# Kernel tuning notes

Hardware: AMD Instinct MI355X
Metric: run time of the kernel (lower is better)

The kernel has to match this reference:

```python
import jax, jax.numpy as jnp
import numpy as np

N = 100000
E = 1600000
NFEAT, NHID1, NHID2, NCLASS, NSTRUC = 512, 256, 128, 40, 128


def glorot(key, shape):
    lim = 1.0 / np.sqrt(shape[0])
    return jax.random.uniform(key, shape, jnp.float32, -lim, lim)


def setup_inputs() -> dict:
    key = jax.random.key(0)
    ks = jax.random.split(key, 12)
    x = jax.random.normal(ks[0], (N, NFEAT), jnp.float32)
    edge_index = jax.random.randint(ks[1], (2, E), 0, N, jnp.int32)
    edge_weight = jax.random.uniform(ks[2], (E,), jnp.float32)
    return {
        "x": x,
        "edge_index": edge_index,
        "edge_weight": edge_weight,
        "W1": glorot(ks[3], (NFEAT, NHID1)), "b1": jnp.zeros((NHID1,), jnp.float32),
        "W2": glorot(ks[4], (NHID1, NHID2)), "b2": jnp.zeros((NHID2,), jnp.float32),
        "W3": glorot(ks[5], (NHID2, NCLASS)), "b3": jnp.zeros((NCLASS,), jnp.float32),
        "We": glorot(ks[6], (NHID1, NSTRUC)), "be": jnp.zeros((NSTRUC,), jnp.float32),
    }


def spmm(edge_index, edge_weight, support):
    # adj @ support with adj given as weighted edge list (dst <- src)
    src, dst = edge_index[0], edge_index[1]
    msgs = support[src] * edge_weight[:, None]  # [E, d]
    return jax.ops.segment_sum(msgs, dst, num_segments=N)


def gc_layer(x, edge_index, edge_weight, W, b):
    support = x @ W
    return spmm(edge_index, edge_weight, support) + b


def reference(x, edge_index, edge_weight, W1, b1, W2, b2, W3, b3, We, be):
    # eval mode: dropout is identity
    h = jax.nn.relu(gc_layer(x, edge_index, edge_weight, W1, b1))
    out1 = jax.nn.relu(gc_layer(h, edge_index, edge_weight, W2, b2))
    out1 = gc_layer(out1, edge_index, edge_weight, W3, b3)
    out2 = h @ We + be
    return jax.nn.log_softmax(out1, axis=1), out2
```

## Files before the change

### kernel.cpp

```cpp
#include <hip/hip_runtime.h>
#include <hip/hip_bf16.h>

#define NNODES 100000
#define NEDGES 1600000
#define BSH 7
#define NBUCK ((NNODES + 127) >> 7)
#define SPBLK 1536
#define P4CHUNK 8192
#define NSCAT ((NEDGES + P4CHUNK - 1) / P4CHUNK)
#define MH1 391

typedef __attribute__((ext_vector_type(8))) short bf16x8;
typedef __attribute__((ext_vector_type(4))) short bf16x4;
typedef __attribute__((ext_vector_type(2))) short bf16x2;
typedef __attribute__((ext_vector_type(4))) float f32x4;
typedef __attribute__((ext_vector_type(2))) float f32x2;

static __device__ __forceinline__ short f2bf(float f) {
  __hip_bfloat16 b = __float2bfloat16(f);
  return __builtin_bit_cast(short, b);
}
static __device__ __forceinline__ float bf2f(short s) {
  unsigned int u = ((unsigned int)(unsigned short)s) << 16;
  return __builtin_bit_cast(float, u);
}
static __device__ __forceinline__ void fma4(f32x4& a, float w, bf16x4 v) {
  a[0] = fmaf(w, bf2f(v[0]), a[0]);
  a[1] = fmaf(w, bf2f(v[1]), a[1]);
  a[2] = fmaf(w, bf2f(v[2]), a[2]);
  a[3] = fmaf(w, bf2f(v[3]), a[3]);
}
static __device__ __forceinline__ void fma2(f32x2& a, float w, bf16x2 v) {
  a[0] = fmaf(w, bf2f(v[0]), a[0]);
  a[1] = fmaf(w, bf2f(v[1]), a[1]);
}

static __device__ __forceinline__ void gload16(const void* g, void* l) {
  __builtin_amdgcn_global_load_lds(
      (const __attribute__((address_space(1))) unsigned int*)g,
      (__attribute__((address_space(3))) unsigned int*)l, 16, 0, 0);
}

static __device__ __forceinline__ void wtrans_body(int blk, const float* __restrict__ W,
                                                   short* __restrict__ Wt,
                                                   int K, int Nvalid, int Npad) {
  int idx = blk * 256 + threadIdx.x;
  if (idx >= Npad * K) return;
  int n = idx / K, k = idx - n * K;
  int ks = (k & ~63) | ((((k >> 3) & 7) ^ (n & 7)) << 3) | (k & 7);
  Wt[idx] = (n < Nvalid) ? f2bf(W[(size_t)ks * Nvalid + n]) : (short)0;
}

static __device__ __forceinline__ void bcount_body(int blk, const int* __restrict__ ei,
                                                   int* __restrict__ bcnt, int* h) {
  for (int i = threadIdx.x; i < NBUCK; i += 256) h[i] = 0;
  __syncthreads();
  for (int e = blk * 256 + threadIdx.x; e < NEDGES; e += 256 * 256)
    atomicAdd(&h[ei[NEDGES + e] >> BSH], 1);
  __syncthreads();
  for (int i = threadIdx.x; i < NBUCK; i += 256)
    if (h[i]) atomicAdd(&bcnt[i], h[i]);
}

static __device__ __forceinline__ void bscatter_body(int blk, int* cnt, int* pos,
                                                     const int* __restrict__ ei,
                                                     const float* __restrict__ ew,
                                                     int* __restrict__ bcur,
                                                     int2* __restrict__ tmp) {
  int tid = threadIdx.x;
  for (int i = tid; i < NBUCK; i += 256) cnt[i] = 0;
  __syncthreads();
  int base = blk * P4CHUNK;
  int end = base + P4CHUNK;
  if (end > NEDGES) end = NEDGES;
  for (int e = base + tid; e < end; e += 256)
    atomicAdd(&cnt[ei[NEDGES + e] >> BSH], 1);
  __syncthreads();
  for (int i = tid; i < NBUCK; i += 256)
    if (cnt[i]) pos[i] = atomicAdd(&bcur[i], cnt[i]);
  __syncthreads();
  for (int e = base + tid; e < end; e += 256) {
    int d = ei[NEDGES + e];
    int b = d >> BSH;
    int p = atomicAdd(&pos[b], 1);
    tmp[p] = make_int2(ei[e] | ((d & 127) << 17), __float_as_int(ew[e]));
  }
}

static __device__ __forceinline__ void bsort_body(int b, int* hist, int* cur,
                                                  const int* __restrict__ bbase,
                                                  const int2* __restrict__ tmp,
                                                  int2* __restrict__ edat,
                                                  int* __restrict__ rowptr) {
  int tid = threadIdx.x;
  int base = bbase[b], cnt = bbase[b + 1] - base;
  if (tid < 128) hist[tid] = 0;
  __syncthreads();
  for (int i = tid; i < cnt; i += 256)
    atomicAdd(&hist[(tmp[base + i].x >> 17) & 127], 1);
  __syncthreads();
  int c = (tid < 128) ? hist[tid] : 0;
  if (tid < 128) cur[tid] = c;
  __syncthreads();
  for (int off = 1; off < 128; off <<= 1) {
    int v = (tid < 128 && tid >= off) ? cur[tid - off] : 0;
    __syncthreads();
    if (tid < 128) cur[tid] += v;
    __syncthreads();
  }
  if (tid < 128) {
    int ex = cur[tid] - c;
    int node = (b << BSH) + tid;
    if (node < NNODES) rowptr[node] = base + ex;
    cur[tid] = base + ex;
  }
  __syncthreads();
  for (int i = tid; i < cnt; i += 256) {
    int2 r = tmp[base + i];
    int d = (r.x >> 17) & 127;
    int p = atomicAdd(&cur[d], 1);
    edat[p] = make_int2(r.x & 0x1FFFF, r.y);
  }
}

__global__ void bscan_kernel(const int* __restrict__ bcnt, int* __restrict__ bbase,
                             int* __restrict__ bcur, int* __restrict__ rowptr) {
  __shared__ int lds[1024];
  int t = threadIdx.x;
  int c = (t < NBUCK) ? bcnt[t] : 0;
  lds[t] = c;
  __syncthreads();
  for (int off = 1; off < 1024; off <<= 1) {
    int v = (t >= off) ? lds[t - off] : 0;
    __syncthreads();
    lds[t] += v;
    __syncthreads();
  }
  if (t < NBUCK) {
    int ex = lds[t] - c;
    bbase[t] = ex;
    bcur[t] = ex;
  }
  if (t == NBUCK) bbase[t] = NEDGES;
  if (t == 0) rowptr[NNODES] = NEDGES;
}

#define LDSTR 72
template <bool AF32, int EPI>
static __device__ void gemm_body(int my, int nx, short* As, short* Bs,
                                 const void* __restrict__ Aptr, int K,
                                 const short* __restrict__ Wt,
                                 void* __restrict__ Cp0, float* __restrict__ Cp1,
                                 const float* __restrict__ bias, int nvalid, int ldc) {
  int tid = threadIdx.x;
  int lane = tid & 63, wv = tid >> 6;
  int wr = wv >> 1, wc = wv & 1;
  int m0 = my * 128;
  int n0 = nx * 128;
  f32x4 acc[4][4];
#pragma unroll
  for (int i = 0; i < 4; i++)
#pragma unroll
    for (int j = 0; j < 4; j++) acc[i][j] = (f32x4){0.f, 0.f, 0.f, 0.f};

  int srow = tid >> 3;
  int scol = (tid & 7) * 8;

  for (int k0 = 0; k0 < K; k0 += 64) {
    if constexpr (AF32) {
#pragma unroll
      for (int p = 0; p < 4; p++) {
        int ml = p * 32 + srow;
        int arow = m0 + ml;
        if (arow >= NNODES) arow = NNODES - 1;
        const float* ap = (const float*)Aptr + (size_t)arow * K + k0 + scol;
        f32x4 a0 = *(const f32x4*)ap;
        f32x4 a1 = *(const f32x4*)(ap + 4);
        bf16x8 av;
#pragma unroll
        for (int j = 0; j < 4; j++) { av[j] = f2bf(a0[j]); av[4 + j] = f2bf(a1[j]); }
        *(bf16x8*)&As[ml * LDSTR + scol] = av;
      }
    } else {
#pragma unroll
      for (int p = 0; p < 4; p++) {
        int row = p * 32 + wv * 8 + (lane >> 3);
        int arow = m0 + row;
        if (arow >= NNODES) arow = NNODES - 1;
        gload16((const short*)Aptr + (size_t)arow * K + k0 + (lane & 7) * 8,
                &As[p * 2048 + wv * 512]);
      }
    }
#pragma unroll
    for (int p = 0; p < 4; p++) {
      int row = p * 32 + wv * 8 + (lane >> 3);
      gload16(Wt + (size_t)(n0 + row) * K + k0 + (lane & 7) * 8,
              &Bs[p * 2048 + wv * 512]);
    }
    __syncthreads();
    int r = lane & 15, quad = lane >> 4;
#pragma unroll
    for (int kk = 0; kk < 64; kk += 32) {
      int csw = (kk + quad * 8) ^ ((r & 7) << 3);
      bf16x8 af[4], bfr[4];
#pragma unroll
      for (int i = 0; i < 4; i++) {
        if constexpr (AF32)
          af[i] = *(const bf16x8*)&As[(wr * 64 + i * 16 + r) * LDSTR + kk + quad * 8];
        else
          af[i] = *(const bf16x8*)&As[((wr * 64 + i * 16 + r) << 6) + csw];
      }
#pragma unroll
      for (int j = 0; j < 4; j++)
        bfr[j] = *(const bf16x8*)&Bs[((wc * 64 + j * 16 + r) << 6) + csw];
#pragma unroll
      for (int i = 0; i < 4; i++)
#pragma unroll
        for (int j = 0; j < 4; j++)
          acc[i][j] = __builtin_amdgcn_mfma_f32_16x16x32_bf16(af[i], bfr[j], acc[i][j], 0, 0, 0);
    }
    __syncthreads();
  }

  int quad = lane >> 4, cl = lane & 15;
#pragma unroll
  for (int i = 0; i < 4; i++) {
    int rowb = m0 + wr * 64 + i * 16 + quad * 4;
#pragma unroll
    for (int rr = 0; rr < 4; rr++) {
      int row = rowb + rr;
      if (row < NNODES) {
#pragma unroll
        for (int j = 0; j < 4; j++) {
          int col = n0 + wc * 64 + j * 16 + cl;
          float v = acc[i][j][rr];
          if (EPI == 0) {
            ((short*)Cp0)[(size_t)row * ldc + col] = f2bf(v);
          } else if (EPI == 1) {
            if (col < nvalid) Cp1[(size_t)row * nvalid + col] = v;
          } else {
            if (col < 128) ((short*)Cp0)[(size_t)row * 128 + col] = f2bf(v);
            else Cp1[(size_t)row * 128 + (col - 128)] = v + bias[col - 128];
          }
        }
      }
    }
  }
}

template <bool AF32, int EPI>
__launch_bounds__(256, 2)
__global__ void gemm_tiled(const void* __restrict__ Aptr, int K,
                           const short* __restrict__ Wt,
                           void* __restrict__ Cp0, float* __restrict__ Cp1,
                           const float* __restrict__ bias, int nvalid, int ldc) {
  __shared__ __align__(16) short As[128 * (AF32 ? LDSTR : 64)];
  __shared__ __align__(16) short Bs[128 * 64];
  gemm_body<AF32, EPI>(blockIdx.y, blockIdx.x, As, Bs, Aptr, K, Wt, Cp0, Cp1, bias, nvalid, ldc);
}

__launch_bounds__(256)
__global__ void front_kernel(const float* __restrict__ W1, short* __restrict__ Wt1,
                             const float* __restrict__ W2, const float* __restrict__ We,
                             short* __restrict__ Wt2e, const float* __restrict__ W3,
                             short* __restrict__ Wt3,
                             const int* __restrict__ ei, int* __restrict__ bcnt) {
  __shared__ int h[NBUCK];
  int b = blockIdx.x;
  if (b < 256) { bcount_body(b, ei, bcnt, h); return; }
  b -= 256;
  if (b < 512) { wtrans_body(b, W1, Wt1, 512, 256, 256); return; }
  b -= 512;
  if (b < 128) { wtrans_body(b, W2, Wt2e, 256, 128, 128); return; }
  b -= 128;
  if (b < 128) { wtrans_body(b, We, Wt2e + (size_t)128 * 256, 256, 128, 128); return; }
  b -= 128;
  wtrans_body(b, W3, Wt3, 128, 40, 128);
}
#define FRONT_BLOCKS (256 + 512 + 128 + 128 + 64)

__launch_bounds__(256, 2)
__global__ void fuseA_kernel(const int* __restrict__ ei, const float* __restrict__ ew,
                             int* __restrict__ bcur, int2* __restrict__ tmp,
                             const float* __restrict__ x, const short* __restrict__ Wt1,
                             short* __restrict__ S1bf) {
  __shared__ __align__(16) short As[128 * LDSTR];
  __shared__ __align__(16) short Bs[128 * 64];
  __shared__ int sc_cnt[NBUCK];
  __shared__ int sc_pos[NBUCK];
  if (blockIdx.x < NSCAT) {
    bscatter_body(blockIdx.x, sc_cnt, sc_pos, ei, ew, bcur, tmp);
  } else {
    int g = blockIdx.x - NSCAT;
    gemm_body<true, 0>(g >> 1, g & 1, As, Bs, x, 512, Wt1, S1bf, nullptr, nullptr, 256, 256);
  }
}

__launch_bounds__(256, 2)
__global__ void fuseB_kernel(const int* __restrict__ bbase, const int2* __restrict__ tmp,
                             int2* __restrict__ edat, int* __restrict__ rowptr,
                             const float* __restrict__ x, const short* __restrict__ Wt1,
                             short* __restrict__ S1bf) {
  __shared__ __align__(16) short As[128 * LDSTR];
  __shared__ __align__(16) short Bs[128 * 64];
  __shared__ int so_hist[128];
  __shared__ int so_cur[128];
  if (blockIdx.x < NBUCK) {
    bsort_body(blockIdx.x, so_hist, so_cur, bbase, tmp, edat, rowptr);
  } else {
    int g = blockIdx.x - NBUCK;
    gemm_body<true, 0>(MH1 + (g >> 1), g & 1, As, Bs, x, 512, Wt1, S1bf, nullptr, nullptr, 256, 256);
  }
}


template <int NE>
static __device__ __forceinline__ void gat1(int2 me, int b, const short* Sc,
                                            f32x4& acc0, f32x4& acc1) {
  int src[NE]; float wt[NE]; bf16x4 v[NE];
#pragma unroll
  for (int j = 0; j < NE; j++) {
    src[j] = __builtin_amdgcn_readlane(me.x, b + j);
    wt[j] = __builtin_bit_cast(float, __builtin_amdgcn_readlane(me.y, b + j));
  }
#pragma unroll
  for (int j = 0; j < NE; j++) v[j] = *(const bf16x4*)(Sc + (size_t)src[j] * 256);
#pragma unroll
  for (int j = 0; j < NE; j++) {
    if (j & 1) fma4(acc1, wt[j], v[j]); else fma4(acc0, wt[j], v[j]);
  }
}

template <int NE>
static __device__ __forceinline__ void gat2(int2 me, int b, const short* Sc,
                                            f32x2& acc0, f32x2& acc1) {
  int src[NE]; float wt[NE]; bf16x2 v[NE];
#pragma unroll
  for (int j = 0; j < NE; j++) {
    src[j] = __builtin_amdgcn_readlane(me.x, b + j);
    wt[j] = __builtin_bit_cast(float, __builtin_amdgcn_readlane(me.y, b + j));
  }
#pragma unroll
  for (int j = 0; j < NE; j++) v[j] = *(const bf16x2*)(Sc + (size_t)src[j] * 128);
#pragma unroll
  for (int j = 0; j < NE; j++) {
    if (j & 1) fma2(acc1, wt[j], v[j]); else fma2(acc0, wt[j], v[j]);
  }
}

template <int NE>
static __device__ __forceinline__ void gat3(int2 me, int b, const float* S3l,
                                            float& acc0, float& acc1) {
  int src[NE]; float wt[NE]; float v[NE];
#pragma unroll
  for (int j = 0; j < NE; j++) {
    src[j] = __builtin_amdgcn_readlane(me.x, b + j);
    wt[j] = __builtin_bit_cast(float, __builtin_amdgcn_readlane(me.y, b + j));
  }
#pragma unroll
  for (int j = 0; j < NE; j++) v[j] = S3l[(size_t)src[j] * 40];
#pragma unroll
  for (int j = 0; j < NE; j++) {
    if (j & 1) acc1 = fmaf(wt[j], v[j], acc1); else acc0 = fmaf(wt[j], v[j], acc0);
  }
}

__launch_bounds__(256, 6)
__global__ void spmm1_kernel(const int* __restrict__ rowptr, const int2* __restrict__ edat,
                             const short* __restrict__ S,
                             const float* __restrict__ bias, short* __restrict__ H) {
  int nw = gridDim.x * 4;
  int wid = blockIdx.x * 4 + (threadIdx.x >> 6);
  int lane = threadIdx.x & 63;
  int c0 = lane * 4;
  const short* Sc = S + c0;
  f32x4 bv = *(const f32x4*)(bias + c0);
  for (int node = wid; node < NNODES; node += nw) {
    f32x4 acc0 = (f32x4){0.f, 0.f, 0.f, 0.f};
    f32x4 acc1 = (f32x4){0.f, 0.f, 0.f, 0.f};
    int beg = rowptr[node], end = rowptr[node + 1];
    for (int w0 = beg; w0 < end; w0 += 64) {
      int wcnt = end - w0;
      if (wcnt > 64) wcnt = 64;
      int2 me = (lane < wcnt) ? edat[w0 + lane] : make_int2(0, 0);
      int g16 = wcnt >> 4, rem = wcnt & 15;
      int b = 0;
      for (int g = 0; g < g16; ++g, b += 16) gat1<16>(me, b, Sc, acc0, acc1);
      if (rem) {
        if (rem > 8) gat1<16>(me, b, Sc, acc0, acc1);
        else gat1<8>(me, b, Sc, acc0, acc1);
      }
    }
    bf16x4 h;
#pragma unroll
    for (int j = 0; j < 4; j++) h[j] = f2bf(fmaxf(acc0[j] + acc1[j] + bv[j], 0.f));
    int c0w = ((lane >> 4) << 6) + ((((lane >> 1) & 7) ^ (node & 7)) << 3) + ((lane & 1) << 2);
    *(bf16x4*)(H + (size_t)node * 256 + c0w) = h;
  }
}

__launch_bounds__(256, 6)
__global__ void spmm2_kernel(const int* __restrict__ rowptr, const int2* __restrict__ edat,
                             const short* __restrict__ S,
                             const float* __restrict__ bias, short* __restrict__ H) {
  int nw = gridDim.x * 4;
  int wid = blockIdx.x * 4 + (threadIdx.x >> 6);
  int lane = threadIdx.x & 63;
  int c0 = lane * 2;
  const short* Sc = S + c0;
  float b0 = bias[c0], b1 = bias[c0 + 1];
  for (int node = wid; node < NNODES; node += nw) {
    f32x2 acc0 = (f32x2){0.f, 0.f};
    f32x2 acc1 = (f32x2){0.f, 0.f};
    int beg = rowptr[node], end = rowptr[node + 1];
    for (int w0 = beg; w0 < end; w0 += 64) {
      int wcnt = end - w0;
      if (wcnt > 64) wcnt = 64;
      int2 me = (lane < wcnt) ? edat[w0 + lane] : make_int2(0, 0);
      int g16 = wcnt >> 4, rem = wcnt & 15;
      int b = 0;
      for (int g = 0; g < g16; ++g, b += 16) gat2<16>(me, b, Sc, acc0, acc1);
      if (rem) {
        if (rem > 8) gat2<16>(me, b, Sc, acc0, acc1);
        else gat2<8>(me, b, Sc, acc0, acc1);
      }
    }
    bf16x2 h;
    h[0] = f2bf(fmaxf(acc0[0] + acc1[0] + b0, 0.f));
    h[1] = f2bf(fmaxf(acc0[1] + acc1[1] + b1, 0.f));
    int c0w = ((lane >> 5) << 6) + ((((lane >> 2) & 7) ^ (node & 7)) << 3) + ((lane & 3) << 1);
    *(bf16x2*)(H + (size_t)node * 128 + c0w) = h;
  }
}

__launch_bounds__(256, 6)
__global__ void spmm3_kernel(const int* __restrict__ rowptr, const int2* __restrict__ edat,
                             const float* __restrict__ S3,
                             const float* __restrict__ b3, float* __restrict__ out1) {
  int nw = gridDim.x * 4;
  int wid = blockIdx.x * 4 + (threadIdx.x >> 6);
  int lane = threadIdx.x & 63;
  bool act = lane < 40;
  const float* S3l = S3 + lane;
  float bl = act ? b3[lane] : 0.f;
  for (int node = wid; node < NNODES; node += nw) {
    float acc0 = 0.f, acc1 = 0.f;
    int beg = rowptr[node], end = rowptr[node + 1];
    for (int w0 = beg; w0 < end; w0 += 64) {
      int wcnt = end - w0;
      if (wcnt > 64) wcnt = 64;
      int2 me = (lane < wcnt) ? edat[w0 + lane] : make_int2(0, 0);
      int g16 = wcnt >> 4, rem = wcnt & 15;
      int b = 0;
      for (int g = 0; g < g16; ++g, b += 16) gat3<16>(me, b, S3l, acc0, acc1);
      if (rem) {
        if (rem > 8) gat3<16>(me, b, S3l, acc0, acc1);
        else gat3<8>(me, b, S3l, acc0, acc1);
      }
    }
    float acc = acc0 + acc1 + bl;
    float v = act ? acc : -__builtin_inff();
    for (int off = 32; off > 0; off >>= 1) v = fmaxf(v, __shfl_xor(v, off));
    float e = act ? expf(acc - v) : 0.f;
    for (int off = 32; off > 0; off >>= 1) e += __shfl_xor(e, off);
    float ls = logf(e);
    if (act) out1[(size_t)node * 40 + lane] = acc - v - ls;
  }
}

extern "C" void kernel_launch(void* const* d_in, const int* in_sizes, int n_in,
                              void* d_out, int out_size, void* d_ws, size_t ws_size,
                              hipStream_t stream) {
  const float* x  = (const float*)d_in[0];
  const int*   ei = (const int*)d_in[1];
  const float* ew = (const float*)d_in[2];
  const float* W1 = (const float*)d_in[3];
  const float* b1 = (const float*)d_in[4];
  const float* W2 = (const float*)d_in[5];
  const float* b2 = (const float*)d_in[6];
  const float* W3 = (const float*)d_in[7];
  const float* b3 = (const float*)d_in[8];
  const float* We = (const float*)d_in[9];
  const float* be = (const float*)d_in[10];
  float* out1 = (float*)d_out;
  float* out2 = (float*)d_out + (size_t)NNODES * 40;

  char* w = (char*)d_ws;
  size_t off = 0;
  auto alloc = [&](size_t bytes) -> char* {
    char* p = w + off;
    off += (bytes + 255) & ~(size_t)255;
    return p;
  };
  int*   rowptr = (int*)alloc((size_t)(NNODES + 1) * 4);
  int*   bcnt   = (int*)alloc((size_t)NBUCK * 4);
  int*   bbase  = (int*)alloc((size_t)(NBUCK + 1) * 4);
  int*   bcur   = (int*)alloc((size_t)NBUCK * 4);
  int2*  edat   = (int2*)alloc((size_t)NEDGES * 8);
  short* Wt1    = (short*)alloc((size_t)256 * 512 * 2);
  short* Wt2e   = (short*)alloc((size_t)256 * 256 * 2);
  short* Wt3    = (short*)alloc((size_t)128 * 128 * 2);
  short* S1bf   = (short*)alloc((size_t)NNODES * 256 * 2);
  short* Hbf    = (short*)alloc((size_t)NNODES * 256 * 2);
  short* S2bf   = (short*)alloc((size_t)NNODES * 128 * 2);
  short* Tbf    = (short*)alloc((size_t)NNODES * 128 * 2);
  float* S3     = (float*)alloc(((size_t)NNODES * 40 + 64) * 4);
  int2*  tmp    = (int2*)S3;

  hipMemsetAsync(bcnt, 0, (size_t)NBUCK * 4, stream);
  front_kernel<<<FRONT_BLOCKS, 256, 0, stream>>>(W1, Wt1, W2, We, Wt2e, W3, Wt3, ei, bcnt);
  bscan_kernel<<<1, 1024, 0, stream>>>(bcnt, bbase, bcur, rowptr);

  fuseA_kernel<<<NSCAT + MH1 * 2, 256, 0, stream>>>(ei, ew, bcur, tmp, x, Wt1, S1bf);
  fuseB_kernel<<<NBUCK + (782 - MH1) * 2, 256, 0, stream>>>(bbase, tmp, edat, rowptr, x, Wt1, S1bf);

  int gblocks = (NNODES + 127) / 128;

  spmm1_kernel<<<SPBLK, 256, 0, stream>>>(rowptr, edat, S1bf, b1, Hbf);
  gemm_tiled<false, 2><<<dim3(2, gblocks), 256, 0, stream>>>(Hbf, 256, Wt2e, S2bf, out2, be, 256, 128);
  spmm2_kernel<<<SPBLK, 256, 0, stream>>>(rowptr, edat, S2bf, b2, Tbf);
  gemm_tiled<false, 1><<<dim3(1, gblocks), 256, 0, stream>>>(Tbf, 128, Wt3, nullptr, S3, nullptr, 40, 40);
  spmm3_kernel<<<SPBLK, 256, 0, stream>>>(rowptr, edat, S3, b3, out1);
}
```

Baseline: 712.3 us.

## Fuse layer-3 GEMM into spmm2 epilogue and overlap spmm1 tail with GEMM2

Removes the separate Tbf intermediate and the small W3 GEMM. Each spmm2 wave now keeps W3 rows in registers and computes the 40-wide S3 row directly from the relu output staged in LDS. spmm1 is also split in two: nodes below N1SPLIT run first, and the remaining nodes are interleaved in one kernel with GEMM2 tiles over the already-finished rows. A final GEMM launch covers the rest. This aims to cut launch count and the Tbf write and read round trip, and to overlap GEMM2 with gather work. The cost is extra register pressure in spmm2 and per-node dot-product work on only 40 of 64 lanes.

After: 1.196 ms. 67.9% more time.

```diff
diff --git a/kernel.cpp b/kernel.cpp
--- a/kernel.cpp
+++ b/kernel.cpp
@@ -9,6 +9,9 @@
 #define P4CHUNK 8192
 #define NSCAT ((NEDGES + P4CHUNK - 1) / P4CHUNK)
 #define MH1 391
+#define MH2 586
+#define N1SPLIT (MH2 * 128)
+#define NSP2 512
 
 typedef __attribute__((ext_vector_type(8))) short bf16x8;
 typedef __attribute__((ext_vector_type(4))) short bf16x4;
@@ -43,11 +46,11 @@
 
 static __device__ __forceinline__ void wtrans_body(int blk, const float* __restrict__ W,
                                                    short* __restrict__ Wt,
-                                                   int K, int Nvalid, int Npad) {
+                                                   int K, int Nvalid, int Npad, int swz) {
   int idx = blk * 256 + threadIdx.x;
   if (idx >= Npad * K) return;
   int n = idx / K, k = idx - n * K;
-  int ks = (k & ~63) | ((((k >> 3) & 7) ^ (n & 7)) << 3) | (k & 7);
+  int ks = swz ? ((k & ~63) | ((((k >> 3) & 7) ^ (n & 7)) << 3) | (k & 7)) : k;
   Wt[idx] = (n < Nvalid) ? f2bf(W[(size_t)ks * Nvalid + n]) : (short)0;
 }
 
@@ -236,8 +239,6 @@
           float v = acc[i][j][rr];
           if (EPI == 0) {
             ((short*)Cp0)[(size_t)row * ldc + col] = f2bf(v);
-          } else if (EPI == 1) {
-            if (col < nvalid) Cp1[(size_t)row * nvalid + col] = v;
           } else {
             if (col < 128) ((short*)Cp0)[(size_t)row * 128 + col] = f2bf(v);
             else Cp1[(size_t)row * 128 + (col - 128)] = v + bias[col - 128];
@@ -253,10 +254,10 @@
 __global__ void gemm_tiled(const void* __restrict__ Aptr, int K,
                            const short* __restrict__ Wt,
                            void* __restrict__ Cp0, float* __restrict__ Cp1,
-                           const float* __restrict__ bias, int nvalid, int ldc) {
+                           const float* __restrict__ bias, int nvalid, int ldc, int my0) {
   __shared__ __align__(16) short As[128 * (AF32 ? LDSTR : 64)];
   __shared__ __align__(16) short Bs[128 * 64];
-  gemm_body<AF32, EPI>(blockIdx.y, blockIdx.x, As, Bs, Aptr, K, Wt, Cp0, Cp1, bias, nvalid, ldc);
+  gemm_body<AF32, EPI>(my0 + blockIdx.y, blockIdx.x, As, Bs, Aptr, K, Wt, Cp0, Cp1, bias, nvalid, ldc);
 }
 
 __launch_bounds__(256)
@@ -269,13 +270,13 @@
   int b = blockIdx.x;
   if (b < 256) { bcount_body(b, ei, bcnt, h); return; }
   b -= 256;
-  if (b < 512) { wtrans_body(b, W1, Wt1, 512, 256, 256); return; }
+  if (b < 512) { wtrans_body(b, W1, Wt1, 512, 256, 256, 1); return; }
   b -= 512;
-  if (b < 128) { wtrans_body(b, W2, Wt2e, 256, 128, 128); return; }
+  if (b < 128) { wtrans_body(b, W2, Wt2e, 256, 128, 128, 1); return; }
   b -= 128;
-  if (b < 128) { wtrans_body(b, We, Wt2e + (size_t)128 * 256, 256, 128, 128); return; }
+  if (b < 128) { wtrans_body(b, We, Wt2e + (size_t)128 * 256, 256, 128, 128, 1); return; }
   b -= 128;
-  wtrans_body(b, W3, Wt3, 128, 40, 128);
+  wtrans_body(b, W3, Wt3, 128, 40, 128, 0);
 }
 #define FRONT_BLOCKS (256 + 512 + 128 + 128 + 64)
 
@@ -365,17 +366,17 @@
   }
 }
 
-__launch_bounds__(256, 6)
-__global__ void spmm1_kernel(const int* __restrict__ rowptr, const int2* __restrict__ edat,
-                             const short* __restrict__ S,
-                             const float* __restrict__ bias, short* __restrict__ H) {
-  int nw = gridDim.x * 4;
-  int wid = blockIdx.x * 4 + (threadIdx.x >> 6);
+static __device__ __forceinline__ void spmm1_body(int wid, int nw, int n0, int n1,
+                                                  const int* __restrict__ rowptr,
+                                                  const int2* __restrict__ edat,
+                                                  const short* __restrict__ S,
+                                                  const float* __restrict__ bias,
+                                                  short* __restrict__ H) {
   int lane = threadIdx.x & 63;
   int c0 = lane * 4;
   const short* Sc = S + c0;
   f32x4 bv = *(const f32x4*)(bias + c0);
-  for (int node = wid; node < NNODES; node += nw) {
+  for (int node = n0 + wid; node < n1; node += nw) {
     f32x4 acc0 = (f32x4){0.f, 0.f, 0.f, 0.f};
     f32x4 acc1 = (f32x4){0.f, 0.f, 0.f, 0.f};
     int beg = rowptr[node], end = rowptr[node + 1];
@@ -400,15 +401,53 @@
 }
 
 __launch_bounds__(256, 6)
+__global__ void spmm1_kernel(const int* __restrict__ rowptr, const int2* __restrict__ edat,
+                             const short* __restrict__ S,
+                             const float* __restrict__ bias, short* __restrict__ H,
+                             int n0, int n1) {
+  spmm1_body(blockIdx.x * 4 + (threadIdx.x >> 6), gridDim.x * 4, n0, n1,
+             rowptr, edat, S, bias, H);
+}
+
+__launch_bounds__(256, 3)
+__global__ void fuse2_kernel(const int* __restrict__ rowptr, const int2* __restrict__ edat,
+                             const short* __restrict__ S1bf, const float* __restrict__ b1,
+                             short* Hbf, const short* __restrict__ Wt2e,
+                             short* __restrict__ S2bf, float* __restrict__ out2,
+                             const float* __restrict__ be) {
+  __shared__ __align__(16) short As[128 * 64];
+  __shared__ __align__(16) short Bs[128 * 64];
+  int bid = blockIdx.x;
+  int idx;
+  bool is_spmm;
+  if (bid < 2 * NSP2) { is_spmm = bid & 1; idx = bid >> 1; }
+  else { is_spmm = false; idx = NSP2 + (bid - 2 * NSP2); }
+  if (is_spmm) {
+    spmm1_body(idx * 4 + (threadIdx.x >> 6), NSP2 * 4, N1SPLIT, NNODES,
+               rowptr, edat, S1bf, b1, Hbf);
+  } else {
+    gemm_body<false, 2>(idx >> 1, idx & 1, As, Bs, Hbf, 256, Wt2e, S2bf, out2, be, 256, 128);
+  }
+}
+#define FUSE2_BLOCKS (2 * NSP2 + (MH2 * 2 - NSP2))
+
+__launch_bounds__(256, 6)
 __global__ void spmm2_kernel(const int* __restrict__ rowptr, const int2* __restrict__ edat,
                              const short* __restrict__ S,
-                             const float* __restrict__ bias, short* __restrict__ H) {
+                             const float* __restrict__ bias,
+                             const short* __restrict__ Wt3, float* __restrict__ S3) {
+  __shared__ float Tl[4][128];
   int nw = gridDim.x * 4;
   int wid = blockIdx.x * 4 + (threadIdx.x >> 6);
+  int wvv = threadIdx.x >> 6;
   int lane = threadIdx.x & 63;
   int c0 = lane * 2;
   const short* Sc = S + c0;
   float b0 = bias[c0], b1 = bias[c0 + 1];
+  bf16x8 wrow[16];
+  const short* wr = Wt3 + (size_t)(lane < 40 ? lane : 0) * 128;
+#pragma unroll
+  for (int j = 0; j < 16; j++) wrow[j] = *(const bf16x8*)(wr + j * 8);
   for (int node = wid; node < NNODES; node += nw) {
     f32x2 acc0 = (f32x2){0.f, 0.f};
     f32x2 acc1 = (f32x2){0.f, 0.f};
@@ -425,11 +464,27 @@
         else gat2<8>(me, b, Sc, acc0, acc1);
       }
     }
-    bf16x2 h;
-    h[0] = f2bf(fmaxf(acc0[0] + acc1[0] + b0, 0.f));
-    h[1] = f2bf(fmaxf(acc0[1] + acc1[1] + b1, 0.f));
-    int c0w = ((lane >> 5) << 6) + ((((lane >> 2) & 7) ^ (node & 7)) << 3) + ((lane & 3) << 1);
-    *(bf16x2*)(H + (size_t)node * 128 + c0w) = h;
+    float t0 = fmaxf(acc0[0] + acc1[0] + b0, 0.f);
+    float t1 = fmaxf(acc0[1] + acc1[1] + b1, 0.f);
+    Tl[wvv][c0] = t0;
+    Tl[wvv][c0 + 1] = t1;
+    asm volatile("s_waitcnt lgkmcnt(0)" ::: "memory");
+    float s = 0.f;
+#pragma unroll
+    for (int j = 0; j < 16; j++) {
+      f32x4 ta = *(const f32x4*)&Tl[wvv][j * 8];
+      f32x4 tb = *(const f32x4*)&Tl[wvv][j * 8 + 4];
+      bf16x8 w8 = wrow[j];
+      s = fmaf(ta[0], bf2f(w8[0]), s);
+      s = fmaf(ta[1], bf2f(w8[1]), s);
+      s = fmaf(ta[2], bf2f(w8[2]), s);
+      s = fmaf(ta[3], bf2f(w8[3]), s);
+      s = fmaf(tb[0], bf2f(w8[4]), s);
+      s = fmaf(tb[1], bf2f(w8[5]), s);
+      s = fmaf(tb[2], bf2f(w8[6]), s);
+      s = fmaf(tb[3], bf2f(w8[7]), s);
+    }
+    if (lane < 40) S3[(size_t)node * 40 + lane] = s;
   }
 }
 
@@ -503,7 +558,6 @@
   short* S1bf   = (short*)alloc((size_t)NNODES * 256 * 2);
   short* Hbf    = (short*)alloc((size_t)NNODES * 256 * 2);
   short* S2bf   = (short*)alloc((size_t)NNODES * 128 * 2);
-  short* Tbf    = (short*)alloc((size_t)NNODES * 128 * 2);
   float* S3     = (float*)alloc(((size_t)NNODES * 40 + 64) * 4);
   int2*  tmp    = (int2*)S3;
 
@@ -514,11 +568,10 @@
   fuseA_kernel<<<NSCAT + MH1 * 2, 256, 0, stream>>>(ei, ew, bcur, tmp, x, Wt1, S1bf);
   fuseB_kernel<<<NBUCK + (782 - MH1) * 2, 256, 0, stream>>>(bbase, tmp, edat, rowptr, x, Wt1, S1bf);
 
-  int gblocks = (NNODES + 127) / 128;
-
-  spmm1_kernel<<<SPBLK, 256, 0, stream>>>(rowptr, edat, S1bf, b1, Hbf);
-  gemm_tiled<false, 2><<<dim3(2, gblocks), 256, 0, stream>>>(Hbf, 256, Wt2e, S2bf, out2, be, 256, 128);
-  spmm2_kernel<<<SPBLK, 256, 0, stream>>>(rowptr, edat, S2bf, b2, Tbf);
-  gemm_tiled<false, 1><<<dim3(1, gblocks), 256, 0, stream>>>(Tbf, 128, Wt3, nullptr, S3, nullptr, 40, 40);
+  spmm1_kernel<<<SPBLK, 256, 0, stream>>>(rowptr, edat, S1bf, b1, Hbf, 0, N1SPLIT);
+  fuse2_kernel<<<FUSE2_BLOCKS, 256, 0, stream>>>(rowptr, edat, S1bf, b1, Hbf, Wt2e, S2bf, out2, be);
+  gemm_tiled<false, 2><<<dim3(2, 782 - MH2), 256, 0, stream>>>(Hbf, 256, Wt2e, S2bf, out2, be, 256, 128, MH2);
+
+  spmm2_kernel<<<SPBLK, 256, 0, stream>>>(rowptr, edat, S2bf, b2, Wt3, S3);
   spmm3_kernel<<<SPBLK, 256, 0, stream>>>(rowptr, edat, S3, b3, out1);
 }
```
